# Optimization experiments

Hardware: AMD Instinct MI355X
Metric: run time of the kernel (lower is better)

## Reference

```python
import jax, jax.numpy as jnp
import numpy as np

B, H, W, C, NH = 4, 128, 128, 192, 6
KD = C // NH          # key/head dim = 32
SCALING = KD ** -0.5


def dwconv5x5(v, kernel, bias):
    # v: (b,h,w,c), depthwise 5x5, stride 1, pad 2. kernel: (5,5,1,c)
    out = jax.lax.conv_general_dilated(
        v, kernel, window_strides=(1, 1), padding=[(2, 2), (2, 2)],
        dimension_numbers=("NHWC", "HWIO", "NHWC"), feature_group_count=C)
    return out + bias


def setup_inputs() -> dict:
    key = jax.random.key(0)
    ks = jax.random.split(key, 13)
    s = C ** -0.5
    return {
        "x": jax.random.normal(ks[0], (B, H, W, C), jnp.float32),
        "mask_h": 0.1 * jax.random.normal(ks[1], (1, NH, H, H), jnp.float32),
        "mask_w": 0.1 * jax.random.normal(ks[2], (1, NH, W, W), jnp.float32),
        "Wq": s * jax.random.normal(ks[3], (C, C), jnp.float32),
        "bq": 0.01 * jax.random.normal(ks[4], (C,), jnp.float32),
        "Wk": s * jax.random.normal(ks[5], (C, C), jnp.float32),
        "bk": 0.01 * jax.random.normal(ks[6], (C,), jnp.float32),
        "Wv": s * jax.random.normal(ks[7], (C, C), jnp.float32),
        "bv": 0.01 * jax.random.normal(ks[8], (C,), jnp.float32),
        "lepe_w": 0.05 * jax.random.normal(ks[9], (5, 5, 1, C), jnp.float32),
        "lepe_b": jnp.zeros((C,), jnp.float32),
        "Wo": s * jax.random.normal(ks[10], (C, C), jnp.float32),
        "bo": jnp.zeros((C,), jnp.float32),
    }


def reference(x, mask_h, mask_w, Wq, bq, Wk, bk, Wv, bv, lepe_w, lepe_b, Wo, bo):
    b, h, w, _ = x.shape
    q = x @ Wq + bq                                   # (b,h,w,c)
    k = (x @ Wk + bk) * SCALING
    v = x @ Wv + bv
    lepe = dwconv5x5(v, lepe_w, lepe_b)               # (b,h,w,c)

    qr = q.reshape(b, h, w, NH, KD)                   # (b,h,w,n,k)
    kr = k.reshape(b, h, w, NH, KD)
    vr = v.reshape(b, h, w, NH, KD)                   # head_dim == KD (factor=1)

    # ---- row (width-axis) attention ----
    # scores: (b,h,n,w,w')
    qk_w = jnp.einsum("bhwnk,bhunk->bhnwu", qr, kr)
    qk_w = qk_w + mask_w[:, None]                     # (1,1,n,w,w) broadcast over h
    attn_w = jax.nn.softmax(qk_w, axis=-1)
    v1 = jnp.einsum("bhnwu,bhund->bhnwd", attn_w, vr)  # (b,h,n,w,d)

    # ---- column (height-axis) attention ----
    # scores: (b,w,n,h,h')
    qk_h = jnp.einsum("bhwnk,bjwnk->bwnhj", qr, kr)
    qk_h = qk_h + mask_h[:, None]                     # (1,1,n,h,h) broadcast over w
    attn_h = jax.nn.softmax(qk_h, axis=-1)
    out = jnp.einsum("bwnhj,bjnwd->bhwnd", attn_h, v1)  # (b,h,w,n,d)

    out = out.reshape(b, h, w, C) + lepe
    return out @ Wo + bo
```

## Files before the change

### kernel.cpp

```cpp
#include <hip/hip_runtime.h>
#include <hip/hip_bf16.h>

#define BB  4
#define HH  128
#define WW  128
#define CC  192
#define NHH 6
#define KDD 32
#define NTOT (BB*HH*WW*CC)
#define SCALING 0.17677669529663687f
#define WMAT_ELE (12*6*64*8)

typedef __hip_bfloat16 bf16;
typedef short bf16x8 __attribute__((ext_vector_type(8)));
typedef unsigned short ushortx4 __attribute__((ext_vector_type(4)));
typedef float floatx4 __attribute__((ext_vector_type(4)));

__device__ __forceinline__ float b2f(bf16 v) { return __bfloat162float(v); }
__device__ __forceinline__ bf16  f2b(float v) { return __float2bfloat16(v); }
__device__ __forceinline__ unsigned short f2bs(float f) {
  union { bf16 b; unsigned short u; } c; c.b = __float2bfloat16(f); return c.u;
}
__device__ __forceinline__ float s2f(short s) {
  union { unsigned u; float f; } c;
  c.u = ((unsigned)(unsigned short)s) << 16; return c.f;
}

__global__ __launch_bounds__(256) void prep_kernel(
    const float* __restrict__ Wq, const float* __restrict__ Wk,
    const float* __restrict__ Wv, const float* __restrict__ Wo,
    unsigned short* __restrict__ Wt) {
  const int idx = blockIdx.x * 256 + threadIdx.x;
  if (idx >= 4 * 12 * 6 * 64) return;
  const int lane = idx & 63;
  int rest = idx >> 6;
  const int kc = rest % 6; rest /= 6;
  const int nt = rest % 12;
  const int mat = rest / 12;
  const int r16 = lane & 15, quad = lane >> 4;
  const float* W = (mat == 0) ? Wq : (mat == 1) ? Wk : (mat == 2) ? Wv : Wo;
  const float sc = (mat == 1) ? SCALING : 1.f;
  bf16x8 t;
  #pragma unroll
  for (int j = 0; j < 8; ++j)
    t[j] = (short)f2bs(W[(kc * 32 + quad * 8 + j) * CC + nt * 16 + r16] * sc);
  *reinterpret_cast<bf16x8*>(&Wt[(size_t)idx * 8]) = t;
}

__global__ __launch_bounds__(256) void qkv_mfma(
    const float* __restrict__ x, const unsigned short* __restrict__ Wt,
    const float* __restrict__ bq, const float* __restrict__ bk,
    const float* __restrict__ bv,
    bf16* __restrict__ q, bf16* __restrict__ k, bf16* __restrict__ v) {
  __shared__ __align__(16) unsigned short Wlds[18432];
  const int tid = threadIdx.x;
  const int l = tid & 63;
  const int r16 = l & 15, quad = l >> 4;
  const int row0 = blockIdx.x * 128 + (tid >> 6) * 32;
  const floatx4 zero = {0.f, 0.f, 0.f, 0.f};
  bf16x8 a[2][6];
  #pragma unroll
  for (int rs = 0; rs < 2; ++rs) {
    const float* xrow = x + (row0 + rs * 16 + r16) * CC;
    #pragma unroll
    for (int kc = 0; kc < 6; ++kc) {
      const float4* p = reinterpret_cast<const float4*>(xrow + kc * 32 + quad * 8);
      float4 u0 = p[0], u1 = p[1];
      bf16x8 t;
      t[0]=f2bs(u0.x); t[1]=f2bs(u0.y); t[2]=f2bs(u0.z); t[3]=f2bs(u0.w);
      t[4]=f2bs(u1.x); t[5]=f2bs(u1.y); t[6]=f2bs(u1.z); t[7]=f2bs(u1.w);
      a[rs][kc] = t;
    }
  }
  for (int mat = 0; mat < 3; ++mat) {
    const unsigned short* Wm = Wt + mat * WMAT_ELE;
    bf16* outp = (mat == 0) ? q : (mat == 1) ? k : v;
    const float* bias = (mat == 0) ? bq : (mat == 1) ? bk : bv;
    const float bscale = (mat == 1) ? SCALING : 1.f;
    for (int hf = 0; hf < 2; ++hf) {
      __syncthreads();
      #pragma unroll
      for (int c = 0; c < 9; ++c) {
        const int ci = c * 256 + tid;
        *reinterpret_cast<bf16x8*>(&Wlds[ci * 8]) =
            *reinterpret_cast<const bf16x8*>(&Wm[hf * 18432 + ci * 8]);
      }
      __syncthreads();
      #pragma unroll
      for (int ntl = 0; ntl < 6; ++ntl) {
        const int nt = hf * 6 + ntl;
        bf16x8 wfr[6];
        #pragma unroll
        for (int kc = 0; kc < 6; ++kc)
          wfr[kc] = *reinterpret_cast<const bf16x8*>(
              &Wlds[((ntl * 6 + kc) * 64 + l) * 8]);
        floatx4 acc0 = zero, acc1 = zero;
        #pragma unroll
        for (int kc = 0; kc < 6; ++kc) {
          acc0 = __builtin_amdgcn_mfma_f32_16x16x32_bf16(wfr[kc], a[0][kc], acc0, 0, 0, 0);
          acc1 = __builtin_amdgcn_mfma_f32_16x16x32_bf16(wfr[kc], a[1][kc], acc1, 0, 0, 0);
        }
        const int col0 = nt * 16 + quad * 4;
        const float4 b4 = *reinterpret_cast<const float4*>(bias + col0);
        ushortx4 s0, s1;
        s0[0] = f2bs(acc0[0] + b4.x * bscale);
        s0[1] = f2bs(acc0[1] + b4.y * bscale);
        s0[2] = f2bs(acc0[2] + b4.z * bscale);
        s0[3] = f2bs(acc0[3] + b4.w * bscale);
        s1[0] = f2bs(acc1[0] + b4.x * bscale);
        s1[1] = f2bs(acc1[1] + b4.y * bscale);
        s1[2] = f2bs(acc1[2] + b4.z * bscale);
        s1[3] = f2bs(acc1[3] + b4.w * bscale);
        *reinterpret_cast<ushortx4*>(&outp[(row0 + r16) * CC + col0]) = s0;
        *reinterpret_cast<ushortx4*>(&outp[(row0 + 16 + r16) * CC + col0]) = s1;
      }
    }
  }
}

__global__ __launch_bounds__(256) void lepe_kernel(
    const bf16* __restrict__ v, const float* __restrict__ kw,
    const float* __restrict__ kb, float* __restrict__ lepe) {
  const int tid = blockIdx.x * 256 + threadIdx.x;
  const int c8 = tid % (CC / 8);
  const int w  = (tid / (CC / 8)) % WW;
  const int h  = (tid / ((CC / 8) * WW)) % HH;
  const int b  = tid / ((CC / 8) * WW * HH);
  const int c0 = c8 * 8;
  const bf16x8 vzero = {0, 0, 0, 0, 0, 0, 0, 0};
  bf16x8 vv[25];
  #pragma unroll
  for (int kh = 0; kh < 5; ++kh) {
    const int hh = h + kh - 2;
    #pragma unroll
    for (int kwi = 0; kwi < 5; ++kwi) {
      const int ww = w + kwi - 2;
      bf16x8 t = vzero;
      if ((unsigned)hh < HH && (unsigned)ww < WW)
        t = *reinterpret_cast<const bf16x8*>(
            v + ((b * HH + hh) * WW + ww) * CC + c0);
      vv[kh * 5 + kwi] = t;
    }
  }
  float acc[8];
  {
    const float4* kbp = reinterpret_cast<const float4*>(kb + c0);
    float4 b0 = kbp[0], b1 = kbp[1];
    acc[0]=b0.x; acc[1]=b0.y; acc[2]=b0.z; acc[3]=b0.w;
    acc[4]=b1.x; acc[5]=b1.y; acc[6]=b1.z; acc[7]=b1.w;
  }
  #pragma unroll
  for (int tap = 0; tap < 25; ++tap) {
    const float4* kp = reinterpret_cast<const float4*>(kw + tap * CC + c0);
    float4 k0 = kp[0], k1 = kp[1];
    const bf16x8 t = vv[tap];
    acc[0] = fmaf(s2f(t[0]), k0.x, acc[0]);
    acc[1] = fmaf(s2f(t[1]), k0.y, acc[1]);
    acc[2] = fmaf(s2f(t[2]), k0.z, acc[2]);
    acc[3] = fmaf(s2f(t[3]), k0.w, acc[3]);
    acc[4] = fmaf(s2f(t[4]), k1.x, acc[4]);
    acc[5] = fmaf(s2f(t[5]), k1.y, acc[5]);
    acc[6] = fmaf(s2f(t[6]), k1.z, acc[6]);
    acc[7] = fmaf(s2f(t[7]), k1.w, acc[7]);
  }
  float4* op = reinterpret_cast<float4*>(lepe + ((b * HH + h) * WW + w) * CC + c0);
  op[0] = make_float4(acc[0], acc[1], acc[2], acc[3]);
  op[1] = make_float4(acc[4], acc[5], acc[6], acc[7]);
}

__global__ __launch_bounds__(64) void attn_mfma_kernel(
    const bf16* __restrict__ qg, const bf16* __restrict__ kg,
    bf16* vbuf, const float* __restrict__ mask,
    const float* __restrict__ lepeadd, const int rstride, const int is_col) {
  __shared__ unsigned short P[16 * 136];
  const int bx = blockIdx.x;
  const int n = bx % NHH;
  const int p = (bx / NHH) % 128;
  const int b = bx / (NHH * 128);
  const int base = is_col ? ((b * HH * WW + p) * CC + n * KDD)
                          : (((b * HH + p) * WW) * CC + n * KDD);
  const int l = threadIdx.x;
  const int r16 = l & 15, quad = l >> 4;
  const float* mbase = mask + n * 128 * 128;
  const floatx4 zero = {0.f, 0.f, 0.f, 0.f};
  const short* vs = (const short*)vbuf;

  bf16x8 kf[8];
  #pragma unroll
  for (int ni = 0; ni < 8; ++ni) {
    kf[ni] = *reinterpret_cast<const bf16x8*>(
        kg + base + (ni * 16 + r16) * rstride + quad * 8);
  }
  bf16x8 vf[4][2];
  #pragma unroll
  for (int s = 0; s < 4; ++s) {
    #pragma unroll
    for (int nj = 0; nj < 2; ++nj) {
      bf16x8 t;
      #pragma unroll
      for (int j = 0; j < 8; ++j) {
        const int key = s * 32 + quad * 8 + j;
        t[j] = vs[base + key * rstride + nj * 16 + r16];
      }
      vf[s][nj] = t;
    }
  }

  for (int mi = 0; mi < 8; ++mi) {
    bf16x8 qf = *reinterpret_cast<const bf16x8*>(
        qg + base + (mi * 16 + r16) * rstride + quad * 8);
    floatx4 S[8];
    #pragma unroll
    for (int ni = 0; ni < 8; ++ni)
      S[ni] = __builtin_amdgcn_mfma_f32_16x16x32_bf16(qf, kf[ni], zero, 0, 0, 0);
    #pragma unroll
    for (int ni = 0; ni < 8; ++ni)
      #pragma unroll
      for (int i = 0; i < 4; ++i)
        S[ni][i] += mbase[(mi * 16 + quad * 4 + i) * 128 + ni * 16 + r16];
    float linv[4], mrow[4];
    #pragma unroll
    for (int i = 0; i < 4; ++i) {
      float m = S[0][i];
      #pragma unroll
      for (int ni = 1; ni < 8; ++ni) m = fmaxf(m, S[ni][i]);
      m = fmaxf(m, __shfl_xor(m, 1));
      m = fmaxf(m, __shfl_xor(m, 2));
      m = fmaxf(m, __shfl_xor(m, 4));
      m = fmaxf(m, __shfl_xor(m, 8));
      mrow[i] = m;
    }
    #pragma unroll
    for (int i = 0; i < 4; ++i) {
      float lsum = 0.f;
      #pragma unroll
      for (int ni = 0; ni < 8; ++ni) {
        const float pv = __expf(S[ni][i] - mrow[i]);
        S[ni][i] = pv;
        lsum += pv;
      }
      lsum += __shfl_xor(lsum, 1);
      lsum += __shfl_xor(lsum, 2);
      lsum += __shfl_xor(lsum, 4);
      lsum += __shfl_xor(lsum, 8);
      linv[i] = 1.f / lsum;
    }
    #pragma unroll
    for (int ni = 0; ni < 8; ++ni)
      #pragma unroll
      for (int i = 0; i < 4; ++i)
        P[(quad * 4 + i) * 136 + ni * 16 + r16] = f2bs(S[ni][i] * linv[i]);
    floatx4 O[2] = {zero, zero};
    #pragma unroll
    for (int s = 0; s < 4; ++s) {
      bf16x8 pf = *reinterpret_cast<const bf16x8*>(
          &P[r16 * 136 + s * 32 + quad * 8]);
      #pragma unroll
      for (int nj = 0; nj < 2; ++nj)
        O[nj] = __builtin_amdgcn_mfma_f32_16x16x32_bf16(pf, vf[s][nj], O[nj], 0, 0, 0);
    }
    #pragma unroll
    for (int nj = 0; nj < 2; ++nj)
      #pragma unroll
      for (int i = 0; i < 4; ++i) {
        const int addr = base + (mi * 16 + quad * 4 + i) * rstride + nj * 16 + r16;
        float val = O[nj][i];
        if (lepeadd) val += lepeadd[addr];
        vbuf[addr] = f2b(val);
      }
  }
}

__global__ __launch_bounds__(256) void proj_mfma(
    const bf16* __restrict__ pre, const unsigned short* __restrict__ Wto,
    const float* __restrict__ bo, float* __restrict__ out) {
  __shared__ __align__(16) unsigned short Wlds[18432];
  const int tid = threadIdx.x;
  const int l = tid & 63;
  const int r16 = l & 15, quad = l >> 4;
  const int row0 = blockIdx.x * 128 + (tid >> 6) * 32;
  const floatx4 zero = {0.f, 0.f, 0.f, 0.f};
  bf16x8 a[2][6];
  #pragma unroll
  for (int rs = 0; rs < 2; ++rs)
    #pragma unroll
    for (int kc = 0; kc < 6; ++kc)
      a[rs][kc] = *reinterpret_cast<const bf16x8*>(
          pre + (row0 + rs * 16 + r16) * CC + kc * 32 + quad * 8);
  for (int hf = 0; hf < 2; ++hf) {
    __syncthreads();
    #pragma unroll
    for (int c = 0; c < 9; ++c) {
      const int ci = c * 256 + tid;
      *reinterpret_cast<bf16x8*>(&Wlds[ci * 8]) =
          *reinterpret_cast<const bf16x8*>(&Wto[hf * 18432 + ci * 8]);
    }
    __syncthreads();
    #pragma unroll
    for (int ntl = 0; ntl < 6; ++ntl) {
      const int nt = hf * 6 + ntl;
      bf16x8 wfr[6];
      #pragma unroll
      for (int kc = 0; kc < 6; ++kc)
        wfr[kc] = *reinterpret_cast<const bf16x8*>(
            &Wlds[((ntl * 6 + kc) * 64 + l) * 8]);
      floatx4 acc0 = zero, acc1 = zero;
      #pragma unroll
      for (int kc = 0; kc < 6; ++kc) {
        acc0 = __builtin_amdgcn_mfma_f32_16x16x32_bf16(wfr[kc], a[0][kc], acc0, 0, 0, 0);
        acc1 = __builtin_amdgcn_mfma_f32_16x16x32_bf16(wfr[kc], a[1][kc], acc1, 0, 0, 0);
      }
      const int col0 = nt * 16 + quad * 4;
      const float4 b4 = *reinterpret_cast<const float4*>(bo + col0);
      float4 s0 = make_float4(acc0[0] + b4.x, acc0[1] + b4.y,
                              acc0[2] + b4.z, acc0[3] + b4.w);
      float4 s1 = make_float4(acc1[0] + b4.x, acc1[1] + b4.y,
                              acc1[2] + b4.z, acc1[3] + b4.w);
      *reinterpret_cast<float4*>(&out[(row0 + r16) * CC + col0]) = s0;
      *reinterpret_cast<float4*>(&out[(row0 + 16 + r16) * CC + col0]) = s1;
    }
  }
}

extern "C" void kernel_launch(void* const* d_in, const int* in_sizes, int n_in,
                              void* d_out, int out_size, void* d_ws, size_t ws_size,
                              hipStream_t stream) {
  const float* x      = (const float*)d_in[0];
  const float* mask_h = (const float*)d_in[1];
  const float* mask_w = (const float*)d_in[2];
  const float* Wq = (const float*)d_in[3];
  const float* bq = (const float*)d_in[4];
  const float* Wk = (const float*)d_in[5];
  const float* bk = (const float*)d_in[6];
  const float* Wv = (const float*)d_in[7];
  const float* bv = (const float*)d_in[8];
  const float* lw = (const float*)d_in[9];
  const float* lb = (const float*)d_in[10];
  const float* Wo = (const float*)d_in[11];
  const float* bo = (const float*)d_in[12];
  float* out = (float*)d_out;

  bf16* q    = (bf16*)d_ws;
  bf16* kbuf = q + NTOT;
  bf16* v    = kbuf + NTOT;
  unsigned short* Wt = (unsigned short*)(v + NTOT);

  prep_kernel<<<(4*12*6*64 + 255)/256, 256, 0, stream>>>(Wq, Wk, Wv, Wo, Wt);
  qkv_mfma<<<(BB*HH*WW)/128, 256, 0, stream>>>(x, Wt, bq, bk, bv, q, kbuf, v);
  lepe_kernel<<<(NTOT/8 + 255)/256, 256, 0, stream>>>(v, lw, lb, out);
  attn_mfma_kernel<<<BB*128*NHH, 64, 0, stream>>>(
      q, kbuf, v, mask_w, nullptr, CC, 0);
  attn_mfma_kernel<<<BB*128*NHH, 64, 0, stream>>>(
      q, kbuf, v, mask_h, out, WW*CC, 1);
  proj_mfma<<<(BB*HH*WW)/128, 256, 0, stream>>>(v, Wt + 3*WMAT_ELE, bo, out);
}
```

Before: 325.4 us.

## Tile depthwise 5x5 lepe conv through shared memory with per-thread row blocking

```diff
diff --git a/kernel.cpp b/kernel.cpp
--- a/kernel.cpp
+++ b/kernel.cpp
@@ -121,51 +121,65 @@
 __global__ __launch_bounds__(256) void lepe_kernel(
     const bf16* __restrict__ v, const float* __restrict__ kw,
     const float* __restrict__ kb, float* __restrict__ lepe) {
-  const int tid = blockIdx.x * 256 + threadIdx.x;
-  const int c8 = tid % (CC / 8);
-  const int w  = (tid / (CC / 8)) % WW;
-  const int h  = (tid / ((CC / 8) * WW)) % HH;
-  const int b  = tid / ((CC / 8) * WW * HH);
-  const int c0 = c8 * 8;
+  __shared__ __align__(16) unsigned short patch[12 * 132 * 8];
+  const int tid = threadIdx.x;
+  const int cg = blockIdx.x % 24;
+  const int hb = (blockIdx.x / 24) % 16;
+  const int b  = blockIdx.x / (24 * 16);
+  const int c0 = cg * 8;
+  const int h0 = hb * 8;
   const bf16x8 vzero = {0, 0, 0, 0, 0, 0, 0, 0};
-  bf16x8 vv[25];
-  #pragma unroll
-  for (int kh = 0; kh < 5; ++kh) {
-    const int hh = h + kh - 2;
-    #pragma unroll
-    for (int kwi = 0; kwi < 5; ++kwi) {
-      const int ww = w + kwi - 2;
-      bf16x8 t = vzero;
-      if ((unsigned)hh < HH && (unsigned)ww < WW)
-        t = *reinterpret_cast<const bf16x8*>(
-            v + ((b * HH + hh) * WW + ww) * CC + c0);
-      vv[kh * 5 + kwi] = t;
-    }
-  }
-  float acc[8];
+  for (int i = tid; i < 12 * 132; i += 256) {
+    const int row = i / 132, col = i % 132;
+    const int gh = h0 + row - 2, gw = col - 2;
+    bf16x8 t = vzero;
+    if ((unsigned)gh < HH && (unsigned)gw < WW)
+      t = *reinterpret_cast<const bf16x8*>(
+          v + ((b * HH + gh) * WW + gw) * CC + c0);
+    *reinterpret_cast<bf16x8*>(&patch[i * 8]) = t;
+  }
+  __syncthreads();
+  const int wo = tid & 127;
+  const int r0 = (tid >> 7) * 4;
+  float acc[4][8];
   {
     const float4* kbp = reinterpret_cast<const float4*>(kb + c0);
     float4 b0 = kbp[0], b1 = kbp[1];
-    acc[0]=b0.x; acc[1]=b0.y; acc[2]=b0.z; acc[3]=b0.w;
-    acc[4]=b1.x; acc[5]=b1.y; acc[6]=b1.z; acc[7]=b1.w;
-  }
-  #pragma unroll
-  for (int tap = 0; tap < 25; ++tap) {
-    const float4* kp = reinterpret_cast<const float4*>(kw + tap * CC + c0);
-    float4 k0 = kp[0], k1 = kp[1];
-    const bf16x8 t = vv[tap];
-    acc[0] = fmaf(s2f(t[0]), k0.x, acc[0]);
-    acc[1] = fmaf(s2f(t[1]), k0.y, acc[1]);
-    acc[2] = fmaf(s2f(t[2]), k0.z, acc[2]);
-    acc[3] = fmaf(s2f(t[3]), k0.w, acc[3]);
-    acc[4] = fmaf(s2f(t[4]), k1.x, acc[4]);
-    acc[5] = fmaf(s2f(t[5]), k1.y, acc[5]);
-    acc[6] = fmaf(s2f(t[6]), k1.z, acc[6]);
-    acc[7] = fmaf(s2f(t[7]), k1.w, acc[7]);
-  }
-  float4* op = reinterpret_cast<float4*>(lepe + ((b * HH + h) * WW + w) * CC + c0);
-  op[0] = make_float4(acc[0], acc[1], acc[2], acc[3]);
-  op[1] = make_float4(acc[4], acc[5], acc[6], acc[7]);
+    #pragma unroll
+    for (int j = 0; j < 4; ++j) {
+      acc[j][0]=b0.x; acc[j][1]=b0.y; acc[j][2]=b0.z; acc[j][3]=b0.w;
+      acc[j][4]=b1.x; acc[j][5]=b1.y; acc[j][6]=b1.z; acc[j][7]=b1.w;
+    }
+  }
+  const unsigned short* pbase = &patch[(r0 * 132 + wo) * 8];
+  for (int kh = 0; kh < 5; ++kh) {
+    #pragma unroll
+    for (int kwi = 0; kwi < 5; ++kwi) {
+      const float4* kp = reinterpret_cast<const float4*>(
+          kw + (kh * 5 + kwi) * CC + c0);
+      float4 k0 = kp[0], k1 = kp[1];
+      #pragma unroll
+      for (int j = 0; j < 4; ++j) {
+        bf16x8 t = *reinterpret_cast<const bf16x8*>(
+            pbase + ((j + kh) * 132 + kwi) * 8);
+        acc[j][0] = fmaf(s2f(t[0]), k0.x, acc[j][0]);
+        acc[j][1] = fmaf(s2f(t[1]), k0.y, acc[j][1]);
+        acc[j][2] = fmaf(s2f(t[2]), k0.z, acc[j][2]);
+        acc[j][3] = fmaf(s2f(t[3]), k0.w, acc[j][3]);
+        acc[j][4] = fmaf(s2f(t[4]), k1.x, acc[j][4]);
+        acc[j][5] = fmaf(s2f(t[5]), k1.y, acc[j][5]);
+        acc[j][6] = fmaf(s2f(t[6]), k1.z, acc[j][6]);
+        acc[j][7] = fmaf(s2f(t[7]), k1.w, acc[j][7]);
+      }
+    }
+  }
+  #pragma unroll
+  for (int j = 0; j < 4; ++j) {
+    float4* op = reinterpret_cast<float4*>(
+        lepe + ((b * HH + h0 + r0 + j) * WW + wo) * CC + c0);
+    op[0] = make_float4(acc[j][0], acc[j][1], acc[j][2], acc[j][3]);
+    op[1] = make_float4(acc[j][4], acc[j][5], acc[j][6], acc[j][7]);
+  }
 }
 
 __global__ __launch_bounds__(64) void attn_mfma_kernel(
@@ -347,7 +361,7 @@
 
   prep_kernel<<<(4*12*6*64 + 255)/256, 256, 0, stream>>>(Wq, Wk, Wv, Wo, Wt);
   qkv_mfma<<<(BB*HH*WW)/128, 256, 0, stream>>>(x, Wt, bq, bk, bv, q, kbuf, v);
-  lepe_kernel<<<(NTOT/8 + 255)/256, 256, 0, stream>>>(v, lw, lb, out);
+  lepe_kernel<<<BB*16*24, 256, 0, stream>>>(v, lw, lb, out);
   attn_mfma_kernel<<<BB*128*NHH, 64, 0, stream>>>(
       q, kbuf, v, mask_w, nullptr, CC, 0);
   attn_mfma_kernel<<<BB*128*NHH, 64, 0, stream>>>(
```

After: 340.1 us. 4.5% more time.
